# Kernel tuning notes

Measured on AMD Instinct MI355X. Metric: run time of the kernel, lower is better.

## Reference

```python
import jax, jax.numpy as jnp
import numpy as np

BATCH, T, IN, HID = 64, 2048, 128, 256

def setup_inputs() -> dict:
    key = jax.random.key(0)
    ks = jax.random.split(key, 6)
    s = 0.05
    return {
        "x": jax.random.normal(ks[0], (BATCH, T, IN), dtype=jnp.float32),
        "w_ih0": jax.random.normal(ks[1], (IN, 4 * HID), dtype=jnp.float32) * s,
        "w_hh0": jax.random.normal(ks[2], (HID, 4 * HID), dtype=jnp.float32) * s,
        "b0": jnp.zeros((4 * HID,), dtype=jnp.float32),
        "w_ih1": jax.random.normal(ks[3], (HID, 4 * HID), dtype=jnp.float32) * s,
        "w_hh1": jax.random.normal(ks[4], (HID, 4 * HID), dtype=jnp.float32) * s,
        "b1": jnp.zeros((4 * HID,), dtype=jnp.float32),
    }

def _run_layer(xs, h0, c0, w_ih, w_hh, b):
    # xs: [T, B, D]. Original code iterates input_[T-1-t], i.e. reversed time.
    def step(carry, xt):
        h, c = carry
        gates = xt @ w_ih + h @ w_hh + b            # [B, 4H]
        f, i, o, g = jnp.split(gates, 4, axis=1)     # split order f,i,o,g as in source
        c1 = jax.nn.sigmoid(f) * c + jax.nn.sigmoid(i) * jnp.tanh(g)
        h1 = jax.nn.sigmoid(o) * jnp.tanh(c1)
        return (h1, c1), h1
    (hT, cT), ys = jax.lax.scan(step, (h0, c0), xs[::-1])
    return ys, hT, cT

def reference(x, w_ih0, w_hh0, b0, w_ih1, w_hh1, b1):
    xs = jnp.transpose(x, (1, 0, 2))                 # batch_first -> [T, B, IN]
    B = xs.shape[1]
    H = w_hh0.shape[0]
    h0 = jnp.zeros((B, H), dtype=xs.dtype)
    # Both layers start from the SAME zero hx (faithful to source).
    y0, hn0, cn0 = _run_layer(xs, h0, h0, w_ih0, w_hh0, b0)
    y1, hn1, cn1 = _run_layer(y0, h0, h0, w_ih1, w_hh1, b1)
    # Source never transposes output back: output is [T, B, H]
    return y1, (jnp.stack([hn0, hn1], 0), jnp.stack([cn0, cn1], 0))
```

## Files before the change

### kernel.cpp

```cpp
#include <hip/hip_runtime.h>
#include <cstdint>
#include <cstddef>

#define T_STEPS 2048
#define NBATCH  64
#define HID     256
#define NGATE   1024

#define KR   192
#define KRC  24
#define KLC  8
#define REC_LDS_BYTES (KLC*1024*16 + 1024)

typedef _Float16 f16x8 __attribute__((ext_vector_type(8)));
typedef _Float16 h2f   __attribute__((ext_vector_type(2)));
typedef float    f32x4 __attribute__((ext_vector_type(4)));

__device__ __forceinline__ unsigned short f2h_bits(float f) {
    _Float16 h = (_Float16)f;
    return __builtin_bit_cast(unsigned short, h);
}
__device__ __forceinline__ float h2f_scalar(unsigned short u) {
    return (float)__builtin_bit_cast(_Float16, u);
}

__device__ __forceinline__ float fdot2u(unsigned int hh, unsigned int ww, float acc) {
#if __has_builtin(__builtin_amdgcn_fdot2)
    return __builtin_amdgcn_fdot2(__builtin_bit_cast(h2f, hh),
                                  __builtin_bit_cast(h2f, ww), acc, false);
#else
    h2f a = __builtin_bit_cast(h2f, hh), b = __builtin_bit_cast(h2f, ww);
    return acc + (float)a.x * (float)b.x + (float)a.y * (float)b.y;
#endif
}

#define OFF_G    ((size_t)0)
#define OFF_Y0   ((size_t)268435456)
#define OFF_WT0  ((size_t)335544320)
#define OFF_WT1  ((size_t)336068608)
#define OFF_LW0  ((size_t)336592896)
#define OFF_LW1  ((size_t)336723968)
#define OFF_BS0  ((size_t)336855040)
#define OFF_BS1  ((size_t)337117184)
#define WS_NEED  ((size_t)337641472)

__global__ void convert_weights(const float* __restrict__ w_ih0, const float* __restrict__ w_hh0,
                                const float* __restrict__ w_ih1, const float* __restrict__ w_hh1,
                                unsigned short* __restrict__ WT0, unsigned short* __restrict__ WT1,
                                unsigned short* __restrict__ LW0, unsigned short* __restrict__ LW1,
                                unsigned short* __restrict__ BS0, unsigned short* __restrict__ BS1)
{
    int gid = blockIdx.x * blockDim.x + threadIdx.x;
    int gsz = gridDim.x * blockDim.x;
    for (int s = gid; s < 1024 * 256; s += gsz) {
        int j = s >> 8, k = s & 255;
        WT0[s] = f2h_bits(w_hh0[k * 1024 + j]);
        WT1[s] = f2h_bits(w_hh1[k * 1024 + j]);
    }
    for (int s = gid; s < KLC * 1024 * 8; s += gsz) {
        int i = s & 7, j = (s >> 3) & 1023, c = s >> 13;
        int k = KR + c * 8 + i;
        LW0[s] = f2h_bits(w_hh0[k * 1024 + j]);
        LW1[s] = f2h_bits(w_hh1[k * 1024 + j]);
    }
    for (int s = gid; s < 131072; s += gsz) {
        int i = s & 7, lane = (s >> 3) & 63, kb = (s >> 9) & 3, n16 = s >> 11;
        int k = kb * 32 + (lane >> 4) * 8 + i;
        int n = n16 * 16 + (lane & 15);
        BS0[s] = f2h_bits(w_ih0[k * 1024 + n]);
    }
    for (int s = gid; s < 262144; s += gsz) {
        int i = s & 7, lane = (s >> 3) & 63, kb = (s >> 9) & 7, n16 = s >> 12;
        int k = kb * 32 + (lane >> 4) * 8 + i;
        int n = n16 * 16 + (lane & 15);
        BS1[s] = f2h_bits(w_ih1[k * 1024 + n]);
    }
}

template <int KB, int LAYER>
__global__ __launch_bounds__(256) void gemm_in(const float* __restrict__ A32,
                                               const unsigned short* __restrict__ A16,
                                               const unsigned short* __restrict__ Bsw,
                                               const float* __restrict__ bias,
                                               unsigned short* __restrict__ Gout)
{
    const int lane = threadIdx.x & 63;
    const int wave = threadIdx.x >> 6;
    const int nblk = blockIdx.x & 15;
    const int rblk = blockIdx.x >> 4;
    const int r0 = rblk * 128 + wave * 32;
    const int quad = lane >> 4, ln = lane & 15;

    f32x4 acc[2][4];
#pragma unroll
    for (int q = 0; q < 4; q++) {
        float bv = bias[(nblk * 4 + q) * 16 + ln];
#pragma unroll
        for (int mt = 0; mt < 2; mt++) {
            acc[mt][q][0] = bv; acc[mt][q][1] = bv; acc[mt][q][2] = bv; acc[mt][q][3] = bv;
        }
    }
    const int ar0 = r0 + ln, ar1 = r0 + 16 + ln;
    size_t aoff0, aoff1;
    if (LAYER == 0) {
        aoff0 = ((size_t)(ar0 & 63) * 2048 + (size_t)(2047 - (ar0 >> 6))) * 128;
        aoff1 = ((size_t)(ar1 & 63) * 2048 + (size_t)(2047 - (ar1 >> 6))) * 128;
    } else {
        aoff0 = ((size_t)(2047 - (ar0 >> 6)) * 64 + (size_t)(ar0 & 63)) * 256;
        aoff1 = ((size_t)(2047 - (ar1 >> 6)) * 64 + (size_t)(ar1 & 63)) * 256;
    }
#pragma unroll
    for (int kb = 0; kb < KB; kb++) {
        const int k0 = kb * 32 + quad * 8;
        f16x8 a0, a1;
        if (LAYER == 0) {
            const float* p0 = A32 + aoff0 + k0;
            const float* p1 = A32 + aoff1 + k0;
            float4 fa = *(const float4*)(p0);
            float4 fb = *(const float4*)(p0 + 4);
            float4 fc = *(const float4*)(p1);
            float4 fd = *(const float4*)(p1 + 4);
            a0[0] = (_Float16)fa.x; a0[1] = (_Float16)fa.y; a0[2] = (_Float16)fa.z; a0[3] = (_Float16)fa.w;
            a0[4] = (_Float16)fb.x; a0[5] = (_Float16)fb.y; a0[6] = (_Float16)fb.z; a0[7] = (_Float16)fb.w;
            a1[0] = (_Float16)fc.x; a1[1] = (_Float16)fc.y; a1[2] = (_Float16)fc.z; a1[3] = (_Float16)fc.w;
            a1[4] = (_Float16)fd.x; a1[5] = (_Float16)fd.y; a1[6] = (_Float16)fd.z; a1[7] = (_Float16)fd.w;
        } else {
            a0 = *(const f16x8*)(A16 + aoff0 + k0);
            a1 = *(const f16x8*)(A16 + aoff1 + k0);
        }
#pragma unroll
        for (int q = 0; q < 4; q++) {
            f16x8 bq = *(const f16x8*)(Bsw + (((size_t)(nblk * 4 + q) * KB + kb) * 64 + lane) * 8);
            acc[0][q] = __builtin_amdgcn_mfma_f32_16x16x32_f16(a0, bq, acc[0][q], 0, 0, 0);
            acc[1][q] = __builtin_amdgcn_mfma_f32_16x16x32_f16(a1, bq, acc[1][q], 0, 0, 0);
        }
    }
#pragma unroll
    for (int mt = 0; mt < 2; mt++)
#pragma unroll
        for (int q = 0; q < 4; q++)
#pragma unroll
            for (int rg = 0; rg < 4; rg++) {
                int row = r0 + mt * 16 + quad * 4 + rg;
                int col = (nblk * 4 + q) * 16 + ln;
                int swz = ((col & 255) << 2) | (col >> 8);
                Gout[(size_t)row * 1024 + swz] = f2h_bits(acc[mt][q][rg]);
            }
}

template <int LAYER>
__global__ __launch_bounds__(512, 2) void lstm_rec(const unsigned short* __restrict__ G,
                                                   const unsigned short* __restrict__ WT,
                                                   const unsigned short* __restrict__ LW,
                                                   unsigned short* __restrict__ Y0,
                                                   float* __restrict__ Out)
{
    extern __shared__ char smem[];
    unsigned short* lds_w  = (unsigned short*)smem;
    unsigned short* lds_h0 = (unsigned short*)(smem + (size_t)KLC * 1024 * 16);
    unsigned short* lds_h1 = lds_h0 + 256;

    const int b = blockIdx.x;
    const int tid = threadIdx.x;
    const int wv = tid >> 6, l = tid & 63;
    const int upper = l >> 5;
    const int m = wv * 32 + (l & 31);
    const int j0 = m + upper * 512;
    const int j1 = j0 + 256;

    uint4 wr0[KRC], wr1[KRC];
    {
        const uint4* p0 = (const uint4*)(WT + (size_t)j0 * 256);
        const uint4* p1 = (const uint4*)(WT + (size_t)j1 * 256);
#pragma unroll
        for (int i = 0; i < KRC; i++) { wr0[i] = p0[i]; wr1[i] = p1[i]; }
    }
    {
        const uint4* src = (const uint4*)LW;
        uint4* dst = (uint4*)lds_w;
        for (int i = tid; i < KLC * 1024; i += 512) dst[i] = src[i];
    }
    if (tid < 256) lds_h0[tid] = 0;
    float c = 0.f, hprev = 0.f;
    __syncthreads();

    const unsigned int* Gb = (const unsigned int*)G + (size_t)b * 512;

    for (int t = 0; t < T_STEPS; ++t) {
        unsigned int gpack = Gb[(size_t)t * 32768 + m * 2 + upper];
        if (t && l < 32) {
            if (LAYER == 0) Y0[((size_t)(t - 1) * 64 + b) * 256 + m] = f2h_bits(hprev);
            else            Out[((size_t)(t - 1) * 64 + b) * 256 + m] = hprev;
        }
        const uint4* hv = (const uint4*)((t & 1) ? lds_h1 : lds_h0);
        float a00 = 0, a01 = 0, a02 = 0, a03 = 0;
        float a10 = 0, a11 = 0, a12 = 0, a13 = 0;
#pragma unroll
        for (int ci = 0; ci < KRC; ++ci) {
            uint4 h4 = hv[ci];
            uint4 w = wr0[ci];
            a00 = fdot2u(h4.x, w.x, a00); a01 = fdot2u(h4.y, w.y, a01);
            a02 = fdot2u(h4.z, w.z, a02); a03 = fdot2u(h4.w, w.w, a03);
            w = wr1[ci];
            a10 = fdot2u(h4.x, w.x, a10); a11 = fdot2u(h4.y, w.y, a11);
            a12 = fdot2u(h4.z, w.z, a12); a13 = fdot2u(h4.w, w.w, a13);
        }
        {
            const uint4* wl = (const uint4*)lds_w;
#pragma unroll
            for (int ci = 0; ci < KLC; ++ci) {
                uint4 h4 = hv[KRC + ci];
                uint4 w = wl[ci * 1024 + j0];
                a00 = fdot2u(h4.x, w.x, a00); a01 = fdot2u(h4.y, w.y, a01);
                a02 = fdot2u(h4.z, w.z, a02); a03 = fdot2u(h4.w, w.w, a03);
                w = wl[ci * 1024 + j1];
                a10 = fdot2u(h4.x, w.x, a10); a11 = fdot2u(h4.y, w.y, a11);
                a12 = fdot2u(h4.z, w.z, a12); a13 = fdot2u(h4.w, w.w, a13);
            }
        }
        float v0 = h2f_scalar((unsigned short)(gpack & 0xffff)) + ((a00 + a01) + (a02 + a03));
        float v1 = h2f_scalar((unsigned short)(gpack >> 16))    + ((a10 + a11) + (a12 + a13));
        float q0 = __shfl_xor(v0, 32, 64);
        float q1 = __shfl_xor(v1, 32, 64);
        float fg = upper ? q0 : v0;
        float ig = upper ? q1 : v1;
        float og = upper ? v0 : q0;
        float gg = upper ? v1 : q1;
        float sf = 1.f / (1.f + __expf(-fg));
        float si = 1.f / (1.f + __expf(-ig));
        float so = 1.f / (1.f + __expf(-og));
        float tg = 1.f - 2.f / (1.f + __expf(2.f * gg));
        c = sf * c + si * tg;
        float tc = 1.f - 2.f / (1.f + __expf(2.f * c));
        float h = so * tc;
        hprev = h;
        unsigned short* hn = (t & 1) ? lds_h0 : lds_h1;
        if (l < 32) hn[m] = f2h_bits(h);
        __syncthreads();
    }
    if (l < 32) {
        if (LAYER == 0) Y0[((size_t)(T_STEPS - 1) * 64 + b) * 256 + m] = f2h_bits(hprev);
        else            Out[((size_t)(T_STEPS - 1) * 64 + b) * 256 + m] = hprev;
        Out[(size_t)33554432 + (size_t)LAYER * 16384 + (size_t)b * 256 + m] = hprev;
        Out[(size_t)33554432 + 32768 + (size_t)LAYER * 16384 + (size_t)b * 256 + m] = c;
    }
}

extern "C" void kernel_launch(void* const* d_in, const int* in_sizes, int n_in,
                              void* d_out, int out_size, void* d_ws, size_t ws_size,
                              hipStream_t stream)
{
    const float* x     = (const float*)d_in[0];
    const float* w_ih0 = (const float*)d_in[1];
    const float* w_hh0 = (const float*)d_in[2];
    const float* b0    = (const float*)d_in[3];
    const float* w_ih1 = (const float*)d_in[4];
    const float* w_hh1 = (const float*)d_in[5];
    const float* b1    = (const float*)d_in[6];
    float* out = (float*)d_out;

    if (ws_size < WS_NEED) return;

    char* ws = (char*)d_ws;
    unsigned short* G   = (unsigned short*)(ws + OFF_G);
    unsigned short* Y0  = (unsigned short*)(ws + OFF_Y0);
    unsigned short* WT0 = (unsigned short*)(ws + OFF_WT0);
    unsigned short* WT1 = (unsigned short*)(ws + OFF_WT1);
    unsigned short* LW0 = (unsigned short*)(ws + OFF_LW0);
    unsigned short* LW1 = (unsigned short*)(ws + OFF_LW1);
    unsigned short* BS0 = (unsigned short*)(ws + OFF_BS0);
    unsigned short* BS1 = (unsigned short*)(ws + OFF_BS1);

    (void)hipFuncSetAttribute(reinterpret_cast<const void*>(&lstm_rec<0>),
                              hipFuncAttributeMaxDynamicSharedMemorySize, REC_LDS_BYTES);
    (void)hipFuncSetAttribute(reinterpret_cast<const void*>(&lstm_rec<1>),
                              hipFuncAttributeMaxDynamicSharedMemorySize, REC_LDS_BYTES);

    convert_weights<<<1024, 256, 0, stream>>>(w_ih0, w_hh0, w_ih1, w_hh1,
                                              WT0, WT1, LW0, LW1, BS0, BS1);
    gemm_in<4, 0><<<16384, 256, 0, stream>>>(x, nullptr, BS0, b0, G);
    lstm_rec<0><<<64, 512, REC_LDS_BYTES, stream>>>(G, WT0, LW0, Y0, out);
    gemm_in<8, 1><<<16384, 256, 0, stream>>>(nullptr, Y0, BS1, b1, G);
    lstm_rec<1><<<64, 512, REC_LDS_BYTES, stream>>>(G, WT1, LW1, Y0, out);
}
```

Before: 8.210 ms.

## Use MFMA for recurrent matvec with register-resident pre-swizzled weights

Replaces the per-thread fdot2 recurrent matvec with 16x16x32 MFMA instructions. The hidden vector is broadcast as the A operand, and only row 0 of each accumulator is used. Recurrent weights are repacked into MFMA B-operand layout: 192 K rows are held in registers (96 f16x8 per lane) and the remaining 64 rows sit in LDS. Blocks shrink to 256 threads so each thread owns one hidden unit, which removes the cross-half shuffle. The cost is heavy register pressure, with a risk of spills, and most MFMA lanes do wasted work since only one of the 16 rows is real.

After: 10.36 ms. +26.1%, slower.

```diff
diff --git a/kernel.cpp b/kernel.cpp
--- a/kernel.cpp
+++ b/kernel.cpp
@@ -7,13 +7,9 @@
 #define HID     256
 #define NGATE   1024
 
-#define KR   192
-#define KRC  24
-#define KLC  8
-#define REC_LDS_BYTES (KLC*1024*16 + 1024)
+#define REC_LDS_BYTES (131072 + 1024)
 
 typedef _Float16 f16x8 __attribute__((ext_vector_type(8)));
-typedef _Float16 h2f   __attribute__((ext_vector_type(2)));
 typedef float    f32x4 __attribute__((ext_vector_type(4)));
 
 __device__ __forceinline__ unsigned short f2h_bits(float f) {
@@ -24,44 +20,41 @@
     return (float)__builtin_bit_cast(_Float16, u);
 }
 
-__device__ __forceinline__ float fdot2u(unsigned int hh, unsigned int ww, float acc) {
-#if __has_builtin(__builtin_amdgcn_fdot2)
-    return __builtin_amdgcn_fdot2(__builtin_bit_cast(h2f, hh),
-                                  __builtin_bit_cast(h2f, ww), acc, false);
-#else
-    h2f a = __builtin_bit_cast(h2f, hh), b = __builtin_bit_cast(h2f, ww);
-    return acc + (float)a.x * (float)b.x + (float)a.y * (float)b.y;
-#endif
-}
-
 #define OFF_G    ((size_t)0)
 #define OFF_Y0   ((size_t)268435456)
-#define OFF_WT0  ((size_t)335544320)
-#define OFF_WT1  ((size_t)336068608)
-#define OFF_LW0  ((size_t)336592896)
-#define OFF_LW1  ((size_t)336723968)
-#define OFF_BS0  ((size_t)336855040)
-#define OFF_BS1  ((size_t)337117184)
-#define WS_NEED  ((size_t)337641472)
+#define OFF_WBR0 ((size_t)335544320)
+#define OFF_WBR1 ((size_t)335937536)
+#define OFF_LWR0 ((size_t)336330752)
+#define OFF_LWR1 ((size_t)336461824)
+#define OFF_BS0  ((size_t)336592896)
+#define OFF_BS1  ((size_t)336855040)
+#define WS_NEED  ((size_t)337379328)
 
 __global__ void convert_weights(const float* __restrict__ w_ih0, const float* __restrict__ w_hh0,
                                 const float* __restrict__ w_ih1, const float* __restrict__ w_hh1,
-                                unsigned short* __restrict__ WT0, unsigned short* __restrict__ WT1,
-                                unsigned short* __restrict__ LW0, unsigned short* __restrict__ LW1,
+                                unsigned short* __restrict__ WBR0, unsigned short* __restrict__ WBR1,
+                                unsigned short* __restrict__ LWR0, unsigned short* __restrict__ LWR1,
                                 unsigned short* __restrict__ BS0, unsigned short* __restrict__ BS1)
 {
     int gid = blockIdx.x * blockDim.x + threadIdx.x;
     int gsz = gridDim.x * blockDim.x;
-    for (int s = gid; s < 1024 * 256; s += gsz) {
-        int j = s >> 8, k = s & 255;
-        WT0[s] = f2h_bits(w_hh0[k * 1024 + j]);
-        WT1[s] = f2h_bits(w_hh1[k * 1024 + j]);
-    }
-    for (int s = gid; s < KLC * 1024 * 8; s += gsz) {
-        int i = s & 7, j = (s >> 3) & 1023, c = s >> 13;
-        int k = KR + c * 8 + i;
-        LW0[s] = f2h_bits(w_hh0[k * 1024 + j]);
-        LW1[s] = f2h_bits(w_hh1[k * 1024 + j]);
+    for (int s = gid; s < 196608; s += gsz) {
+        int i = s & 7, lane = (s >> 3) & 63, r = s >> 9;
+        int c = r % 6, t2 = r / 6;
+        int tl = t2 & 15, ww = t2 >> 4;
+        int tig = (tl >> 2) * 16 + ww * 4 + (tl & 3);
+        int n = tig * 16 + (lane & 15);
+        int k = c * 32 + ((lane >> 4) << 3) + i;
+        WBR0[s] = f2h_bits(w_hh0[k * 1024 + n]);
+        WBR1[s] = f2h_bits(w_hh1[k * 1024 + n]);
+    }
+    for (int s = gid; s < 65536; s += gsz) {
+        int i = s & 7, lane = (s >> 3) & 63, r = s >> 9;
+        int cc = r & 1, tig = r >> 1;
+        int n = tig * 16 + (lane & 15);
+        int k = 192 + cc * 32 + ((lane >> 4) << 3) + i;
+        LWR0[s] = f2h_bits(w_hh0[k * 1024 + n]);
+        LWR1[s] = f2h_bits(w_hh1[k * 1024 + n]);
     }
     for (int s = gid; s < 131072; s += gsz) {
         int i = s & 7, lane = (s >> 3) & 63, kb = (s >> 9) & 3, n16 = s >> 11;
@@ -149,101 +142,111 @@
 }
 
 template <int LAYER>
-__global__ __launch_bounds__(512, 2) void lstm_rec(const unsigned short* __restrict__ G,
-                                                   const unsigned short* __restrict__ WT,
-                                                   const unsigned short* __restrict__ LW,
+__global__ __launch_bounds__(256, 1) void lstm_rec(const unsigned short* __restrict__ G,
+                                                   const unsigned short* __restrict__ WBR,
+                                                   const unsigned short* __restrict__ LWR,
                                                    unsigned short* __restrict__ Y0,
                                                    float* __restrict__ Out)
 {
     extern __shared__ char smem[];
     unsigned short* lds_w  = (unsigned short*)smem;
-    unsigned short* lds_h0 = (unsigned short*)(smem + (size_t)KLC * 1024 * 16);
+    unsigned short* lds_h0 = (unsigned short*)(smem + 131072);
     unsigned short* lds_h1 = lds_h0 + 256;
 
     const int b = blockIdx.x;
     const int tid = threadIdx.x;
-    const int wv = tid >> 6, l = tid & 63;
-    const int upper = l >> 5;
-    const int m = wv * 32 + (l & 31);
-    const int j0 = m + upper * 512;
-    const int j1 = j0 + 256;
-
-    uint4 wr0[KRC], wr1[KRC];
+    const int w = tid >> 6, lane = tid & 63;
+    const int quad = lane >> 4;
+    const int m = w * 64 + lane;
+
+    f16x8 wb[6][16];
+#pragma unroll
+    for (int tl = 0; tl < 16; tl++)
+#pragma unroll
+        for (int c = 0; c < 6; c++)
+            wb[c][tl] = *(const f16x8*)(WBR + ((((size_t)w * 16 + tl) * 6 + c) * 64 + lane) * 8);
+
     {
-        const uint4* p0 = (const uint4*)(WT + (size_t)j0 * 256);
-        const uint4* p1 = (const uint4*)(WT + (size_t)j1 * 256);
-#pragma unroll
-        for (int i = 0; i < KRC; i++) { wr0[i] = p0[i]; wr1[i] = p1[i]; }
-    }
-    {
-        const uint4* src = (const uint4*)LW;
+        const uint4* src = (const uint4*)LWR;
         uint4* dst = (uint4*)lds_w;
-        for (int i = tid; i < KLC * 1024; i += 512) dst[i] = src[i];
-    }
-    if (tid < 256) lds_h0[tid] = 0;
-    float c = 0.f, hprev = 0.f;
+        for (int i = tid; i < 8192; i += 256) dst[i] = src[i];
+    }
+    lds_h0[tid] = 0;
+    float c_state = 0.f, hprev = 0.f;
     __syncthreads();
 
-    const unsigned int* Gb = (const unsigned int*)G + (size_t)b * 512;
+    const unsigned short* Gp = G + (size_t)b * 1024 + (size_t)m * 4;
 
     for (int t = 0; t < T_STEPS; ++t) {
-        unsigned int gpack = Gb[(size_t)t * 32768 + m * 2 + upper];
-        if (t && l < 32) {
+        uint2 gpk = *(const uint2*)(Gp + (size_t)t * 65536);
+        if (t) {
             if (LAYER == 0) Y0[((size_t)(t - 1) * 64 + b) * 256 + m] = f2h_bits(hprev);
             else            Out[((size_t)(t - 1) * 64 + b) * 256 + m] = hprev;
         }
-        const uint4* hv = (const uint4*)((t & 1) ? lds_h1 : lds_h0);
-        float a00 = 0, a01 = 0, a02 = 0, a03 = 0;
-        float a10 = 0, a11 = 0, a12 = 0, a13 = 0;
-#pragma unroll
-        for (int ci = 0; ci < KRC; ++ci) {
-            uint4 h4 = hv[ci];
-            uint4 w = wr0[ci];
-            a00 = fdot2u(h4.x, w.x, a00); a01 = fdot2u(h4.y, w.y, a01);
-            a02 = fdot2u(h4.z, w.z, a02); a03 = fdot2u(h4.w, w.w, a03);
-            w = wr1[ci];
-            a10 = fdot2u(h4.x, w.x, a10); a11 = fdot2u(h4.y, w.y, a11);
-            a12 = fdot2u(h4.z, w.z, a12); a13 = fdot2u(h4.w, w.w, a13);
-        }
+        const unsigned short* hcur = (t & 1) ? lds_h1 : lds_h0;
+        uint4 hq[8];
+#pragma unroll
+        for (int c = 0; c < 8; c++)
+            hq[c] = *(const uint4*)(hcur + c * 32 + quad * 8);
+
+        f32x4 acc[16];
         {
-            const uint4* wl = (const uint4*)lds_w;
-#pragma unroll
-            for (int ci = 0; ci < KLC; ++ci) {
-                uint4 h4 = hv[KRC + ci];
-                uint4 w = wl[ci * 1024 + j0];
-                a00 = fdot2u(h4.x, w.x, a00); a01 = fdot2u(h4.y, w.y, a01);
-                a02 = fdot2u(h4.z, w.z, a02); a03 = fdot2u(h4.w, w.w, a03);
-                w = wl[ci * 1024 + j1];
-                a10 = fdot2u(h4.x, w.x, a10); a11 = fdot2u(h4.y, w.y, a11);
-                a12 = fdot2u(h4.z, w.z, a12); a13 = fdot2u(h4.w, w.w, a13);
+            f16x8 a0 = __builtin_bit_cast(f16x8, hq[0]);
+            f32x4 zero = {0.f, 0.f, 0.f, 0.f};
+#pragma unroll
+            for (int tl = 0; tl < 16; tl++)
+                acc[tl] = __builtin_amdgcn_mfma_f32_16x16x32_f16(a0, wb[0][tl], zero, 0, 0, 0);
+        }
+#pragma unroll
+        for (int c = 1; c < 6; c++) {
+            f16x8 a = __builtin_bit_cast(f16x8, hq[c]);
+#pragma unroll
+            for (int tl = 0; tl < 16; tl++)
+                acc[tl] = __builtin_amdgcn_mfma_f32_16x16x32_f16(a, wb[c][tl], acc[tl], 0, 0, 0);
+        }
+#pragma unroll
+        for (int cc = 0; cc < 2; cc++) {
+            f16x8 a = __builtin_bit_cast(f16x8, hq[6 + cc]);
+#pragma unroll
+            for (int tl = 0; tl < 16; tl++) {
+                int g = tl >> 2, u = tl & 3;
+                int tig = g * 16 + w * 4 + u;
+                f16x8 bq = *(const f16x8*)(lds_w + (((size_t)tig * 2 + cc) * 64 + lane) * 8);
+                acc[tl] = __builtin_amdgcn_mfma_f32_16x16x32_f16(a, bq, acc[tl], 0, 0, 0);
             }
         }
-        float v0 = h2f_scalar((unsigned short)(gpack & 0xffff)) + ((a00 + a01) + (a02 + a03));
-        float v1 = h2f_scalar((unsigned short)(gpack >> 16))    + ((a10 + a11) + (a12 + a13));
-        float q0 = __shfl_xor(v0, 32, 64);
-        float q1 = __shfl_xor(v1, 32, 64);
-        float fg = upper ? q0 : v0;
-        float ig = upper ? q1 : v1;
-        float og = upper ? v0 : q0;
-        float gg = upper ? v1 : q1;
+        float fg, ig, og, gg;
+        {
+            float x0, x1, x2, x3, lo, hi;
+            x0 = acc[0][0];  x1 = acc[1][0];  x2 = acc[2][0];  x3 = acc[3][0];
+            lo = (quad & 1) ? x1 : x0; hi = (quad & 1) ? x3 : x2; fg = (quad & 2) ? hi : lo;
+            x0 = acc[4][0];  x1 = acc[5][0];  x2 = acc[6][0];  x3 = acc[7][0];
+            lo = (quad & 1) ? x1 : x0; hi = (quad & 1) ? x3 : x2; ig = (quad & 2) ? hi : lo;
+            x0 = acc[8][0];  x1 = acc[9][0];  x2 = acc[10][0]; x3 = acc[11][0];
+            lo = (quad & 1) ? x1 : x0; hi = (quad & 1) ? x3 : x2; og = (quad & 2) ? hi : lo;
+            x0 = acc[12][0]; x1 = acc[13][0]; x2 = acc[14][0]; x3 = acc[15][0];
+            lo = (quad & 1) ? x1 : x0; hi = (quad & 1) ? x3 : x2; gg = (quad & 2) ? hi : lo;
+        }
+        fg += h2f_scalar((unsigned short)(gpk.x & 0xffff));
+        ig += h2f_scalar((unsigned short)(gpk.x >> 16));
+        og += h2f_scalar((unsigned short)(gpk.y & 0xffff));
+        gg += h2f_scalar((unsigned short)(gpk.y >> 16));
         float sf = 1.f / (1.f + __expf(-fg));
         float si = 1.f / (1.f + __expf(-ig));
         float so = 1.f / (1.f + __expf(-og));
         float tg = 1.f - 2.f / (1.f + __expf(2.f * gg));
-        c = sf * c + si * tg;
-        float tc = 1.f - 2.f / (1.f + __expf(2.f * c));
+        c_state = sf * c_state + si * tg;
+        float tc = 1.f - 2.f / (1.f + __expf(2.f * c_state));
         float h = so * tc;
         hprev = h;
         unsigned short* hn = (t & 1) ? lds_h0 : lds_h1;
-        if (l < 32) hn[m] = f2h_bits(h);
+        hn[m] = f2h_bits(h);
         __syncthreads();
     }
-    if (l < 32) {
-        if (LAYER == 0) Y0[((size_t)(T_STEPS - 1) * 64 + b) * 256 + m] = f2h_bits(hprev);
-        else            Out[((size_t)(T_STEPS - 1) * 64 + b) * 256 + m] = hprev;
-        Out[(size_t)33554432 + (size_t)LAYER * 16384 + (size_t)b * 256 + m] = hprev;
-        Out[(size_t)33554432 + 32768 + (size_t)LAYER * 16384 + (size_t)b * 256 + m] = c;
-    }
+    if (LAYER == 0) Y0[((size_t)(T_STEPS - 1) * 64 + b) * 256 + m] = f2h_bits(hprev);
+    else            Out[((size_t)(T_STEPS - 1) * 64 + b) * 256 + m] = hprev;
+    Out[(size_t)33554432 + (size_t)LAYER * 16384 + (size_t)b * 256 + m] = hprev;
+    Out[(size_t)33554432 + 32768 + (size_t)LAYER * 16384 + (size_t)b * 256 + m] = c_state;
 }
 
 extern "C" void kernel_launch(void* const* d_in, const int* in_sizes, int n_in,
@@ -262,14 +265,14 @@
     if (ws_size < WS_NEED) return;
 
     char* ws = (char*)d_ws;
-    unsigned short* G   = (unsigned short*)(ws + OFF_G);
-    unsigned short* Y0  = (unsigned short*)(ws + OFF_Y0);
-    unsigned short* WT0 = (unsigned short*)(ws + OFF_WT0);
-    unsigned short* WT1 = (unsigned short*)(ws + OFF_WT1);
-    unsigned short* LW0 = (unsigned short*)(ws + OFF_LW0);
-    unsigned short* LW1 = (unsigned short*)(ws + OFF_LW1);
-    unsigned short* BS0 = (unsigned short*)(ws + OFF_BS0);
-    unsigned short* BS1 = (unsigned short*)(ws + OFF_BS1);
+    unsigned short* G    = (unsigned short*)(ws + OFF_G);
+    unsigned short* Y0   = (unsigned short*)(ws + OFF_Y0);
+    unsigned short* WBR0 = (unsigned short*)(ws + OFF_WBR0);
+    unsigned short* WBR1 = (unsigned short*)(ws + OFF_WBR1);
+    unsigned short* LWR0 = (unsigned short*)(ws + OFF_LWR0);
+    unsigned short* LWR1 = (unsigned short*)(ws + OFF_LWR1);
+    unsigned short* BS0  = (unsigned short*)(ws + OFF_BS0);
+    unsigned short* BS1  = (unsigned short*)(ws + OFF_BS1);
 
     (void)hipFuncSetAttribute(reinterpret_cast<const void*>(&lstm_rec<0>),
                               hipFuncAttributeMaxDynamicSharedMemorySize, REC_LDS_BYTES);
@@ -277,9 +280,9 @@
                               hipFuncAttributeMaxDynamicSharedMemorySize, REC_LDS_BYTES);
 
     convert_weights<<<1024, 256, 0, stream>>>(w_ih0, w_hh0, w_ih1, w_hh1,
-                                              WT0, WT1, LW0, LW1, BS0, BS1);
+                                              WBR0, WBR1, LWR0, LWR1, BS0, BS1);
     gemm_in<4, 0><<<16384, 256, 0, stream>>>(x, nullptr, BS0, b0, G);
-    lstm_rec<0><<<64, 512, REC_LDS_BYTES, stream>>>(G, WT0, LW0, Y0, out);
+    lstm_rec<0><<<64, 256, REC_LDS_BYTES, stream>>>(G, WBR0, LWR0, Y0, out);
     gemm_in<8, 1><<<16384, 256, 0, stream>>>(nullptr, Y0, BS1, b1, G);
-    lstm_rec<1><<<64, 512, REC_LDS_BYTES, stream>>>(G, WT1, LW1, Y0, out);
-}
+    lstm_rec<1><<<64, 256, REC_LDS_BYTES, stream>>>(G, WBR1, LWR1, Y0, out);
+}
```
